# Kernel optimization log

Measured on AMD Instinct MI355X. Metric: run time of the kernel, lower is better.

The kernel has to match this reference:

```python
import jax, jax.numpy as jnp
import numpy as np

B, N_NODES, VOCAB, H = 128, 1023, 2048, 256  # depth-9 perfect binary trees (heap layout)


def setup_inputs() -> dict:
    key = jax.random.key(0)
    k1, k2, k3, k4, k5 = jax.random.split(key, 5)
    tokens = jax.random.randint(k1, (B, N_NODES), 0, VOCAB)
    emb = jax.random.normal(k2, (VOCAB, H), dtype=jnp.float32) * 0.02
    Wx = jax.random.normal(k3, (H, 5 * H), dtype=jnp.float32) * 0.02
    Ul = jax.random.normal(k4, (H, 5 * H), dtype=jnp.float32) * 0.02
    Ur = jax.random.normal(k5, (H, 5 * H), dtype=jnp.float32) * 0.02
    b = jnp.zeros((5 * H,), dtype=jnp.float32)
    return {"tokens": tokens, "emb": emb, "Wx": Wx, "Ul": Ul, "Ur": Ur, "b": b}


def _tree_lstm(tokens, emb, Wx, Ul, Ur, b):
    # tokens: [B, 2^(D+1)-1] in level-order heap layout; children of heap index i
    # are 2i+1, 2i+2 -> within level d+1 they sit at offsets 2k, 2k+1.
    n_nodes = tokens.shape[1]
    depth = int(np.log2(n_nodes + 1)) - 1
    hdim = emb.shape[1]
    x_all = emb[tokens]  # [B, N, H] embedding lookup (memory-bound gather)
    h = c = None
    for d in range(depth, -1, -1):  # bottom-up over levels (fixed structural loop)
        start, n = 2 ** d - 1, 2 ** d
        x = x_all[:, start:start + n]  # [B, n, H]
        gates = jnp.einsum('bnh,hg->bng', x, Wx) + b
        if h is not None:
            hl, hr = h[:, 0::2], h[:, 1::2]
            cl, cr = c[:, 0::2], c[:, 1::2]
            gates = gates + jnp.einsum('bnh,hg->bng', hl, Ul) + jnp.einsum('bnh,hg->bng', hr, Ur)
        i, fl, fr, o, u = jnp.split(gates, 5, axis=-1)
        i, fl, fr, o = map(jax.nn.sigmoid, (i, fl, fr, o))
        u = jnp.tanh(u)
        c_new = i * u
        if c is not None:
            c_new = c_new + fl * cl + fr * cr
        c = c_new
        h = o * jnp.tanh(c)
    return h[:, 0], c[:, 0]  # root states, each [B, H]


def reference(tokens, emb, Wx, Ul, Ur, b):
    h_root, _ = _tree_lstm(tokens, emb, Wx, Ul, Ur, b)
    return h_root  # [B, H]
```

## Files before the change

kernel.cpp:

```cpp
#include <hip/hip_runtime.h>
#include <hip/hip_bf16.h>
#include <math.h>

#define B_SZ   128
#define HDIM   256
#define NG     1280
#define NNODES 1023
#define VOCAB  2048

typedef unsigned int uint32;
typedef short  short8v  __attribute__((ext_vector_type(8)));
typedef float  float4v  __attribute__((ext_vector_type(4)));

__device__ __forceinline__ float sigm(float x) {
    return 1.0f / (1.0f + __expf(-x));
}
__device__ __forceinline__ float tanh_fast(float x) {
    return 2.0f / (1.0f + __expf(-2.0f * x)) - 1.0f;
}
__device__ __forceinline__ float bf2f(unsigned short u) {
    return __uint_as_float(((uint32)u) << 16);
}
__device__ __forceinline__ unsigned short f2bf(float f) {
    uint32 x = __float_as_uint(f);
    uint32 r = (x + 0x7FFFu + ((x >> 16) & 1u)) >> 16;
    return (unsigned short)r;
}

__device__ __forceinline__ void dma16(const unsigned short* gptr, unsigned short* lptr) {
    __builtin_amdgcn_global_load_lds(
        (const __attribute__((address_space(1))) void*)gptr,
        (__attribute__((address_space(3))) void*)lptr, 16, 0, 0);
}

__global__ __launch_bounds__(256) void embb_kernel(
    const float* __restrict__ emb, unsigned short* __restrict__ embb)
{
    const int t = blockIdx.x * 256 + threadIdx.x;
    const float4 v0 = *(const float4*)(emb + (size_t)t * 8);
    const float4 v1 = *(const float4*)(emb + (size_t)t * 8 + 4);
    short8v o;
    o[0] = (short)f2bf(v0.x); o[1] = (short)f2bf(v0.y);
    o[2] = (short)f2bf(v0.z); o[3] = (short)f2bf(v0.w);
    o[4] = (short)f2bf(v1.x); o[5] = (short)f2bf(v1.y);
    o[6] = (short)f2bf(v1.z); o[7] = (short)f2bf(v1.w);
    *(short8v*)(embb + (size_t)t * 8) = o;
}

__global__ __launch_bounds__(256) void prep_wtf(
    const float* __restrict__ Ul, const float* __restrict__ Ur,
    const float* __restrict__ Wx, unsigned short* __restrict__ WTf)
{
    const int t = blockIdx.x * 256 + threadIdx.x;
    const int l = t & 63;
    const int q = l >> 4, c = l & 15;
    const int ks = (t >> 6) % 24;
    const int ng = t / (24 * 64);
    const int col = ng * 16 + c;
    const int k = ks * 32 + q * 8;
    const float* src = (k < 256) ? (Ul + (size_t)k * NG + col)
                     : (k < 512) ? (Ur + (size_t)(k - 256) * NG + col)
                                 : (Wx + (size_t)(k - 512) * NG + col);
    short8v v;
    #pragma unroll
    for (int j = 0; j < 8; ++j) v[j] = (short)f2bf(src[(size_t)j * NG]);
    *(short8v*)(WTf + (size_t)t * 8) = v;
}

template <bool TAB, int RT>
__global__ __launch_bounds__(256, 2) void gemm_tab(
    const unsigned short* __restrict__ WTf, const unsigned short* __restrict__ A,
    const float* __restrict__ bias, unsigned short* __restrict__ O0,
    unsigned short* __restrict__ O1,
    unsigned short* __restrict__ Hleaf, unsigned short* __restrict__ Cleaf,
    const int ks_base0)
{
    constexpr int M   = RT * 16;
    constexpr int CPW = RT / 2 ? RT / 2 : 1;
    __shared__ __align__(16) unsigned short Ab[2][RT * 1024];
    __shared__ __align__(16) unsigned short wbE[RT * 5120];

    const int tid  = threadIdx.x;
    const int lane = tid & 63;
    const int w    = tid >> 6;
    const int quad = lane >> 4, col15 = lane & 15;
    const int jt = blockIdx.x;
    const int rowBase = blockIdx.y * M;
    const int jbase   = jt * 64;
    const int ks_base = ks_base0 + (int)blockIdx.z * 8;
    unsigned short* O = blockIdx.z ? O1 : O0;

    const unsigned short* agp[CPW];
    unsigned short* ldst[CPW];
    #pragma unroll
    for (int t = 0; t < CPW; ++t) {
        const int ch = CPW * w + t, sub = ch / RT, rt = ch % RT;
        const int srow = rowBase + rt * 16 + col15;
        agp[t]  = A + (size_t)srow * HDIM + sub * 32 + quad * 8;
        ldst[t] = &Ab[0][0] + ch * 512;
    }

    const short8v* WTfv = (const short8v*)WTf;
    uint32 boff[5];
    #pragma unroll
    for (int g = 0; g < 5; ++g)
        boff[g] = (uint32)(((g * 16 + jt * 4 + w) * 24 + ks_base) * 64 + lane);

    float4v acc[RT][5];
    #pragma unroll
    for (int rt = 0; rt < RT; ++rt)
        #pragma unroll
        for (int g = 0; g < 5; ++g)
            #pragma unroll
            for (int e = 0; e < 4; ++e) acc[rt][g][e] = 0.0f;

    #pragma unroll
    for (int t = 0; t < CPW; ++t) dma16(agp[t], ldst[t]);
    __syncthreads();

    #pragma unroll
    for (int s = 0; s < 4; ++s) {
        if (s < 3) {
            #pragma unroll
            for (int t = 0; t < CPW; ++t)
                dma16(agp[t] + (s + 1) * 64, ldst[t] + ((s + 1) & 1) * (RT * 1024));
        }
        #pragma unroll
        for (int sub = 0; sub < 2; ++sub) {
            short8v bf[5];
            #pragma unroll
            for (int g = 0; g < 5; ++g) bf[g] = WTfv[boff[g] + (s * 2 + sub) * 64];
            #pragma unroll
            for (int rt = 0; rt < RT; ++rt) {
                const short8v af = *(const short8v*)&Ab[s & 1][(sub * RT + rt) * 512 + lane * 8];
                #pragma unroll
                for (int g = 0; g < 5; ++g)
                    acc[rt][g] = __builtin_amdgcn_mfma_f32_16x16x32_bf16(
                        af, bf[g], acc[rt][g], 0, 0, 0);
            }
        }
        __syncthreads();
    }

    const int jl = w * 16 + col15;
    const int j  = jbase + jl;
    float bz[5];
    #pragma unroll
    for (int g = 0; g < 5; ++g) bz[g] = bias ? bias[g * 256 + j] : 0.0f;
    const int jchunk = jl >> 3, jpos = jl & 7;

    if (TAB) {
        #pragma unroll
        for (int rt = 0; rt < RT; ++rt) {
            #pragma unroll
            for (int reg = 0; reg < 4; ++reg) {
                const int rr = rt * 16 + quad * 4 + reg;
                const float gi = acc[rt][0][reg] + bz[0];
                const float go = acc[rt][3][reg] + bz[3];
                const float gu = acc[rt][4][reg] + bz[4];
                const float c = sigm(gi) * tanh_fast(gu);
                const float h = sigm(go) * tanh_fast(c);
                Hleaf[(size_t)(rowBase + rr) * HDIM + j] = f2bf(h);
                Cleaf[(size_t)(rowBase + rr) * HDIM + j] = f2bf(c);
            }
        }
    }

    #pragma unroll
    for (int rt = 0; rt < RT; ++rt) {
        #pragma unroll
        for (int reg = 0; reg < 4; ++reg) {
            const int rr = rt * 16 + quad * 4 + reg;
            const int roff = ((jchunk + 2 * quad) & 7) * 8 + jpos;
            #pragma unroll
            for (int g = 0; g < 5; ++g)
                wbE[(g * M + rr) * 64 + roff] = f2bf(acc[rt][g][reg] + bz[g]);
        }
    }
    __syncthreads();

    #pragma unroll
    for (int k2 = 0; k2 < RT * 5 / 2; ++k2) {
        const int c = tid + k2 * 256;
        const int g = c / (M * 8), rr = (c >> 3) & (M - 1), u = c & 7;
        const int ru = (u + 2 * ((rr >> 2) & 3)) & 7;
        const short8v v = *(const short8v*)&wbE[(g * M + rr) * 64 + ru * 8];
        *(short8v*)(O + (size_t)(rowBase + rr) * NG + g * 256 + jbase + u * 8) = v;
    }
}

__global__ __launch_bounds__(256) void leafcell_kernel(
    const int* __restrict__ tokens,
    const unsigned short* __restrict__ HUl, const unsigned short* __restrict__ HUr,
    const unsigned short* __restrict__ EWb, const unsigned short* __restrict__ Cleaf,
    unsigned short* __restrict__ hdst, unsigned short* __restrict__ cdst)
{
    const int t = blockIdx.x * 256 + threadIdx.x;
    const int row = t >> 4;
    const int j0  = (t & 15) * 8;
    const int b = row >> 8, i = row & 255;
    const int tokN = tokens[b * NNODES + 255 + i];
    const int tokL = tokens[b * NNODES + 511 + 2 * i];
    const int tokR = tokens[b * NNODES + 512 + 2 * i];

    const unsigned short* pl = HUl + (size_t)tokL * NG + j0;
    const unsigned short* pr = HUr + (size_t)tokR * NG + j0;
    const unsigned short* pn = EWb + (size_t)tokN * NG + j0;

    float g5[5][2][8];
    #pragma unroll
    for (int g = 0; g < 5; ++g) {
        #pragma unroll
        for (int h2 = 0; h2 < 2; ++h2) {
            const short8v vl = *(const short8v*)(pl + g * 256 + h2 * 128);
            const short8v vr = *(const short8v*)(pr + g * 256 + h2 * 128);
            const short8v vn = *(const short8v*)(pn + g * 256 + h2 * 128);
            #pragma unroll
            for (int e = 0; e < 8; ++e)
                g5[g][h2][e] = bf2f((unsigned short)vl[e]) + bf2f((unsigned short)vr[e])
                             + bf2f((unsigned short)vn[e]);
        }
    }
    #pragma unroll
    for (int h2 = 0; h2 < 2; ++h2) {
        const short8v cl8 = *(const short8v*)(Cleaf + (size_t)tokL * HDIM + j0 + h2 * 128);
        const short8v cr8 = *(const short8v*)(Cleaf + (size_t)tokR * HDIM + j0 + h2 * 128);
        short8v ho, co;
        #pragma unroll
        for (int e = 0; e < 8; ++e) {
            const float ii = sigm(g5[0][h2][e]), fl = sigm(g5[1][h2][e]);
            const float fr = sigm(g5[2][h2][e]), oo = sigm(g5[3][h2][e]);
            const float uu = tanh_fast(g5[4][h2][e]);
            const float c = ii * uu + fl * bf2f((unsigned short)cl8[e])
                                    + fr * bf2f((unsigned short)cr8[e]);
            const float h = oo * tanh_fast(c);
            co[e] = (short)f2bf(c);
            ho[e] = (short)f2bf(h);
        }
        *(short8v*)(hdst + (size_t)row * HDIM + j0 + h2 * 128) = ho;
        *(short8v*)(cdst + (size_t)row * HDIM + j0 + h2 * 128) = co;
    }
}

template <bool SWZ>
__global__ __launch_bounds__(256, 1) void level_fold(
    const unsigned short* __restrict__ WTf, const int* __restrict__ tokens,
    const unsigned short* __restrict__ embb,
    const unsigned short* __restrict__ hsrc, const unsigned short* __restrict__ csrc,
    const float* __restrict__ bias,
    unsigned short* __restrict__ hdst, unsigned short* __restrict__ cdst,
    float* __restrict__ out, const int d)
{
    const int n = 1 << d;

    __shared__ __align__(16) unsigned short Ab[2][16384];

    const int tid  = threadIdx.x;
    const int lane = tid & 63;
    const int w    = tid >> 6;
    const int quad = lane >> 4, col15 = lane & 15;

    int jt, rowTile;
    if (SWZ) {
        const int L = blockIdx.x;
        jt      = (L >> 3) & 3;
        rowTile = (L >> 5) * 8 + (L & 7);
    } else {
        jt      = blockIdx.y;
        rowTile = blockIdx.x;
    }
    const int rowBase = rowTile * 64;
    const int jbase   = jt * 64;

    uint32 oL[4], oN[4];
    #pragma unroll
    for (int t = 0; t < 4; ++t) {
        const int srow = rowBase + t * 16 + col15;
        const int b = srow >> d, i = srow & (n - 1);
        oN[t] = (uint32)tokens[b * NNODES + (n - 1) + i] * 512u + (uint32)(quad * 16);
        oL[t] = (uint32)(2 * srow) * 512u + (uint32)(quad * 16);
    }
    const char* hb = (const char*)hsrc;
    const char* xb = (const char*)embb;

    const short8v* WTfv = (const short8v*)WTf;
    uint32 boff[5];
    #pragma unroll
    for (int g = 0; g < 5; ++g)
        boff[g] = ((g * 16 + jt * 4 + w) * 24) * 64 + lane;

    const int jl = w * 16 + col15;
    const int j  = jbase + jl;
    float bz[5];
    #pragma unroll
    for (int g = 0; g < 5; ++g) bz[g] = bias[g * 256 + j];

    float4v acc[4][5];
    #pragma unroll
    for (int rt = 0; rt < 4; ++rt)
        #pragma unroll
        for (int g = 0; g < 5; ++g)
            #pragma unroll
            for (int e = 0; e < 4; ++e) acc[rt][g][e] = 0.0f;

    {
        #pragma unroll
        for (int t = 0; t < 8; ++t) {
            const int sub = 2 * w + (t >> 2), rt = t & 3;
            dma16((const unsigned short*)(hb + oL[rt] + sub * 64),
                  &Ab[0][0] + (sub * 4 + rt) * 512);
        }
    }
    __syncthreads();

    #pragma unroll
    for (int s = 0; s < 3; ++s) {
        if (s < 2) {
            unsigned short* dstb = &Ab[(s + 1) & 1][0];
            #pragma unroll
            for (int t = 0; t < 8; ++t) {
                const int sub = 2 * w + (t >> 2), rt = t & 3;
                const char* p = (s == 0) ? (hb + oL[rt] + 512 + sub * 64)
                                         : (xb + oN[rt] + sub * 64);
                dma16((const unsigned short*)p, dstb + (sub * 4 + rt) * 512);
            }
        }
        #pragma unroll
        for (int sub = 0; sub < 8; ++sub) {
            short8v bf[5];
            #pragma unroll
            for (int g = 0; g < 5; ++g) bf[g] = WTfv[boff[g] + (s * 8 + sub) * 64];
            #pragma unroll
            for (int rt = 0; rt < 4; ++rt) {
                const short8v af = *(const short8v*)&Ab[s & 1][(sub * 4 + rt) * 512 + lane * 8];
                #pragma unroll
                for (int g = 0; g < 5; ++g)
                    acc[rt][g] = __builtin_amdgcn_mfma_f32_16x16x32_bf16(
                        af, bf[g], acc[rt][g], 0, 0, 0);
            }
        }
        __syncthreads();
    }

    float hv[4][4], cv[4][4];
    #pragma unroll
    for (int rt = 0; rt < 4; ++rt) {
        #pragma unroll
        for (int reg = 0; reg < 4; ++reg) {
            const int rr = rt * 16 + quad * 4 + reg;
            const int grow = rowBase + rr;
            const float cl = bf2f(csrc[(size_t)(2 * grow) * HDIM + j]);
            const float cr = bf2f(csrc[(size_t)(2 * grow + 1) * HDIM + j]);
            const float gi  = acc[rt][0][reg] + bz[0];
            const float gfl = acc[rt][1][reg] + bz[1];
            const float gfr = acc[rt][2][reg] + bz[2];
            const float go  = acc[rt][3][reg] + bz[3];
            const float gu  = acc[rt][4][reg] + bz[4];
            const float ii = sigm(gi), fl = sigm(gfl), fr = sigm(gfr), oo = sigm(go);
            const float uu = tanh_fast(gu);
            const float c = ii * uu + fl * cl + fr * cr;
            const float h = oo * tanh_fast(c);
            cv[rt][reg] = c; hv[rt][reg] = h;
            if (d == 0) out[(size_t)grow * HDIM + j] = h;
        }
    }
    if (d == 0) return;

    unsigned short* wb = &Ab[0][0];
    const int jchunk = jl >> 3, jpos = jl & 7;
    #pragma unroll
    for (int rt = 0; rt < 4; ++rt) {
        #pragma unroll
        for (int reg = 0; reg < 4; ++reg) {
            const int rr = rt * 16 + quad * 4 + reg;
            const int roff = ((jchunk + 2 * quad) & 7) * 8 + jpos;
            wb[rr * 64 + roff]        = f2bf(hv[rt][reg]);
            wb[4096 + rr * 64 + roff] = f2bf(cv[rt][reg]);
        }
    }
    __syncthreads();
    #pragma unroll
    for (int k2 = 0; k2 < 4; ++k2) {
        const int c = tid + k2 * 256;
        const int arr = c >> 9, rr = (c >> 3) & 63, u = c & 7;
        const int ru = (u + 2 * ((rr >> 2) & 3)) & 7;
        const short8v v = *(const short8v*)(wb + (arr * 4096 + rr * 64 + ru * 8));
        unsigned short* dstp = (arr ? cdst : hdst) +
            (size_t)(rowBase + rr) * HDIM + jbase + u * 8;
        *(short8v*)dstp = v;
    }
}

extern "C" void kernel_launch(void* const* d_in, const int* in_sizes, int n_in,
                              void* d_out, int out_size, void* d_ws, size_t ws_size,
                              hipStream_t stream)
{
    const int*   tokens = (const int*)d_in[0];
    const float* emb    = (const float*)d_in[1];
    const float* Wx     = (const float*)d_in[2];
    const float* Ul     = (const float*)d_in[3];
    const float* Ur     = (const float*)d_in[4];
    const float* bias   = (const float*)d_in[5];
    float* out = (float*)d_out;

    const size_t EW_ELEMS  = (size_t)VOCAB * NG;
    const size_t EMB_ELEMS = (size_t)VOCAB * HDIM;
    const size_t WTF_ELEMS = (size_t)80 * 24 * 64 * 8;
    const size_t LT_ELEMS  = (size_t)VOCAB * HDIM;
    const size_t SLOT_A    = (size_t)16384 * HDIM;
    const size_t SLOT_B    = (size_t)32768 * HDIM;
    const size_t REQUIRED  = (3 * EW_ELEMS + EMB_ELEMS + WTF_ELEMS + 2 * LT_ELEMS
                              + 2 * (SLOT_A + SLOT_B)) * 2;
    if (ws_size < REQUIRED || d_ws == nullptr) return;

    char* ws = (char*)d_ws;
    unsigned short* EWb   = (unsigned short*)ws;
    unsigned short* HUl   = EWb + EW_ELEMS;
    unsigned short* HUr   = HUl + EW_ELEMS;
    unsigned short* embb  = HUr + EW_ELEMS;
    unsigned short* WTf   = embb + EMB_ELEMS;
    unsigned short* Hleaf = WTf + WTF_ELEMS;
    unsigned short* Cleaf = Hleaf + LT_ELEMS;
    unsigned short* hA    = Cleaf + LT_ELEMS;
    unsigned short* cA    = hA + SLOT_A;
    unsigned short* hB    = cA + SLOT_A;
    unsigned short* cB    = hB + SLOT_B;

    embb_kernel<<<dim3(256), 256, 0, stream>>>(emb, embb);
    prep_wtf<<<dim3(480), 256, 0, stream>>>(Ul, Ur, Wx, WTf);
    gemm_tab<true, 2><<<dim3(4, 64, 1), 256, 0, stream>>>(
        WTf, embb, bias, EWb, nullptr, Hleaf, Cleaf, 16);
    gemm_tab<false, 2><<<dim3(4, 64, 2), 256, 0, stream>>>(
        WTf, Hleaf, nullptr, HUl, HUr, nullptr, nullptr, 0);

    leafcell_kernel<<<dim3(2048), 256, 0, stream>>>(
        tokens, HUl, HUr, EWb, Cleaf, hB, cB);

    level_fold<true><<<dim3(4 * 256), 256, 0, stream>>>(
        WTf, tokens, embb, hB, cB, bias, hA, cA, out, 7);

    for (int d = 6; d >= 0; --d) {
        const int NRB = 2 << d;
        const bool evenD = ((d & 1) == 0);
        const unsigned short* hs = evenD ? hA : hB;
        const unsigned short* cs = evenD ? cA : cB;
        unsigned short* hd = evenD ? hB : hA;
        unsigned short* cd = evenD ? cB : cA;
        level_fold<false><<<dim3(NRB, 4), 256, 0, stream>>>(
            WTf, tokens, embb, hs, cs, bias, hd, cd, out, d);
    }
}
```

Baseline: 319.0 us.

## Add 128-row tile level_fold8 kernel for the two widest tree levels

Adds a level_fold8 kernel in which each block processes 128 rows (8 row tiles) instead of 64. Each loaded weight fragment is reused across twice as many MFMA row tiles, halving weight traffic per row and the block count. It is used for levels 7 and 6, while smaller levels keep the original 64-row kernel, which is now non-templated. The cost is much higher register pressure (40 float4 accumulators) and an epilogue that writes h and c back in two halves through shared memory, which adds syncs.

New measurement: 499.9 us. 56.7% more time.

```diff
diff --git a/kernel.cpp b/kernel.cpp
--- a/kernel.cpp
+++ b/kernel.cpp
@@ -243,13 +243,13 @@
 }
 
 template <bool SWZ>
-__global__ __launch_bounds__(256, 1) void level_fold(
+__global__ __launch_bounds__(256, 1) void level_fold8(
     const unsigned short* __restrict__ WTf, const int* __restrict__ tokens,
     const unsigned short* __restrict__ embb,
     const unsigned short* __restrict__ hsrc, const unsigned short* __restrict__ csrc,
     const float* __restrict__ bias,
     unsigned short* __restrict__ hdst, unsigned short* __restrict__ cdst,
-    float* __restrict__ out, const int d)
+    const int d)
 {
     const int n = 1 << d;
 
@@ -269,6 +269,149 @@
         jt      = blockIdx.y;
         rowTile = blockIdx.x;
     }
+    const int rowBase = rowTile * 128;
+    const int jbase   = jt * 64;
+
+    const uint32 inrow = (uint32)(w * 64 + quad * 16);
+    uint32 oL[8], oN[8];
+    #pragma unroll
+    for (int t = 0; t < 8; ++t) {
+        const int srow = rowBase + t * 16 + col15;
+        const int b = srow >> d, i = srow & (n - 1);
+        oN[t] = (uint32)tokens[b * NNODES + (n - 1) + i] * 512u + inrow;
+        oL[t] = (uint32)(2 * srow) * 512u + inrow;
+    }
+    const char* hb = (const char*)hsrc;
+    const char* xb = (const char*)embb;
+
+    const short8v* WTfv = (const short8v*)WTf;
+    uint32 boff[5];
+    #pragma unroll
+    for (int g = 0; g < 5; ++g)
+        boff[g] = ((g * 16 + jt * 4 + w) * 24) * 64 + lane;
+
+    const int jl = w * 16 + col15;
+    const int j  = jbase + jl;
+    float bz[5];
+    #pragma unroll
+    for (int g = 0; g < 5; ++g) bz[g] = bias[g * 256 + j];
+
+    float4v acc[8][5];
+    #pragma unroll
+    for (int rt = 0; rt < 8; ++rt)
+        #pragma unroll
+        for (int g = 0; g < 5; ++g)
+            #pragma unroll
+            for (int e = 0; e < 4; ++e) acc[rt][g][e] = 0.0f;
+
+    {
+        unsigned short* dst = &Ab[0][0] + w * 8 * 512;
+        #pragma unroll
+        for (int t = 0; t < 8; ++t)
+            dma16((const unsigned short*)(hb + oL[t]), dst + t * 512);
+    }
+    __syncthreads();
+
+    #pragma unroll
+    for (int s = 0; s < 6; ++s) {
+        if (s < 5) {
+            const int sn = s + 1;
+            unsigned short* dst = &Ab[sn & 1][0] + w * 8 * 512;
+            #pragma unroll
+            for (int t = 0; t < 8; ++t) {
+                const char* p = (sn < 2) ? (hb + oL[t] + sn * 256)
+                              : (sn < 4) ? (hb + oL[t] + 512 + (sn - 2) * 256)
+                                         : (xb + oN[t] + (sn - 4) * 256);
+                dma16((const unsigned short*)p, dst + t * 512);
+            }
+        }
+        #pragma unroll
+        for (int sub = 0; sub < 4; ++sub) {
+            short8v bf[5];
+            #pragma unroll
+            for (int g = 0; g < 5; ++g) bf[g] = WTfv[boff[g] + (s * 4 + sub) * 64];
+            #pragma unroll
+            for (int rt = 0; rt < 8; ++rt) {
+                const short8v af = *(const short8v*)&Ab[s & 1][(sub * 8 + rt) * 512 + lane * 8];
+                #pragma unroll
+                for (int g = 0; g < 5; ++g)
+                    acc[rt][g] = __builtin_amdgcn_mfma_f32_16x16x32_bf16(
+                        af, bf[g], acc[rt][g], 0, 0, 0);
+            }
+        }
+        __syncthreads();
+    }
+
+    unsigned short* wb = &Ab[0][0];
+    const int jchunk = jl >> 3, jpos = jl & 7;
+    #pragma unroll
+    for (int hh = 0; hh < 2; ++hh) {
+        float hv[4][4], cv[4][4];
+        #pragma unroll
+        for (int rt4 = 0; rt4 < 4; ++rt4) {
+            const int rt = hh * 4 + rt4;
+            #pragma unroll
+            for (int reg = 0; reg < 4; ++reg) {
+                const int rr = rt * 16 + quad * 4 + reg;
+                const int grow = rowBase + rr;
+                const float cl = bf2f(csrc[(size_t)(2 * grow) * HDIM + j]);
+                const float cr = bf2f(csrc[(size_t)(2 * grow + 1) * HDIM + j]);
+                const float gi  = acc[rt][0][reg] + bz[0];
+                const float gfl = acc[rt][1][reg] + bz[1];
+                const float gfr = acc[rt][2][reg] + bz[2];
+                const float go  = acc[rt][3][reg] + bz[3];
+                const float gu  = acc[rt][4][reg] + bz[4];
+                const float ii = sigm(gi), fl = sigm(gfl), fr = sigm(gfr), oo = sigm(go);
+                const float uu = tanh_fast(gu);
+                const float c = ii * uu + fl * cl + fr * cr;
+                const float h = oo * tanh_fast(c);
+                cv[rt4][reg] = c; hv[rt4][reg] = h;
+            }
+        }
+        __syncthreads();
+        #pragma unroll
+        for (int rt4 = 0; rt4 < 4; ++rt4) {
+            #pragma unroll
+            for (int reg = 0; reg < 4; ++reg) {
+                const int rr = rt4 * 16 + quad * 4 + reg;
+                const int roff = ((jchunk + 2 * quad) & 7) * 8 + jpos;
+                wb[rr * 64 + roff]        = f2bf(hv[rt4][reg]);
+                wb[4096 + rr * 64 + roff] = f2bf(cv[rt4][reg]);
+            }
+        }
+        __syncthreads();
+        #pragma unroll
+        for (int k2 = 0; k2 < 4; ++k2) {
+            const int c = tid + k2 * 256;
+            const int arr = c >> 9, rr = (c >> 3) & 63, u = c & 7;
+            const int ru = (u + 2 * ((rr >> 2) & 3)) & 7;
+            const short8v v = *(const short8v*)(wb + (arr * 4096 + rr * 64 + ru * 8));
+            unsigned short* dstp = (arr ? cdst : hdst) +
+                (size_t)(rowBase + hh * 64 + rr) * HDIM + jbase + u * 8;
+            *(short8v*)dstp = v;
+        }
+    }
+}
+
+__global__ __launch_bounds__(256, 1) void level_fold(
+    const unsigned short* __restrict__ WTf, const int* __restrict__ tokens,
+    const unsigned short* __restrict__ embb,
+    const unsigned short* __restrict__ hsrc, const unsigned short* __restrict__ csrc,
+    const float* __restrict__ bias,
+    unsigned short* __restrict__ hdst, unsigned short* __restrict__ cdst,
+    float* __restrict__ out, const int d)
+{
+    const int n = 1 << d;
+
+    __shared__ __align__(16) unsigned short Ab[2][16384];
+
+    const int tid  = threadIdx.x;
+    const int lane = tid & 63;
+    const int w    = tid >> 6;
+    const int quad = lane >> 4, col15 = lane & 15;
+
+    const int jt      = blockIdx.y;
+    const int rowTile = blockIdx.x;
     const int rowBase = rowTile * 64;
     const int jbase   = jt * 64;
 
@@ -436,17 +579,19 @@
     leafcell_kernel<<<dim3(2048), 256, 0, stream>>>(
         tokens, HUl, HUr, EWb, Cleaf, hB, cB);
 
-    level_fold<true><<<dim3(4 * 256), 256, 0, stream>>>(
-        WTf, tokens, embb, hB, cB, bias, hA, cA, out, 7);
-
-    for (int d = 6; d >= 0; --d) {
+    level_fold8<true><<<dim3(512), 256, 0, stream>>>(
+        WTf, tokens, embb, hB, cB, bias, hA, cA, 7);
+    level_fold8<false><<<dim3(64, 4), 256, 0, stream>>>(
+        WTf, tokens, embb, hA, cA, bias, hB, cB, 6);
+
+    for (int d = 5; d >= 0; --d) {
         const int NRB = 2 << d;
         const bool evenD = ((d & 1) == 0);
         const unsigned short* hs = evenD ? hA : hB;
         const unsigned short* cs = evenD ? cA : cB;
         unsigned short* hd = evenD ? hB : hA;
         unsigned short* cd = evenD ? cB : cA;
-        level_fold<false><<<dim3(NRB, 4), 256, 0, stream>>>(
+        level_fold<<<dim3(NRB, 4), 256, 0, stream>>>(
             WTf, tokens, embb, hs, cs, bias, hd, cd, out, d);
     }
 }
```
